# Optimization experiments

Hardware: AMD Instinct MI355X
Metric: run time of the kernel (lower is better)

The kernel has to match this reference:

```python
import jax, jax.numpy as jnp
import numpy as np

V, E, H, L, B, T = 32000, 256, 512, 2, 32, 64
SOS_TOKEN = 1


def setup_inputs() -> dict:
    key = jax.random.key(0)
    ks = jax.random.split(key, 16)
    s = 0.02
    inp = {
        'encoder_outputs': jax.random.normal(ks[0], (B, T, H), dtype=jnp.float32),
        'encoder_hidden': jax.random.normal(ks[1], (L, B, H), dtype=jnp.float32),
        'target_tensor': jax.random.randint(ks[2], (B, T), 0, V, dtype=jnp.int64),
        'embedding': jax.random.normal(ks[3], (V, E), dtype=jnp.float32) * s,
        'W_ih0': jax.random.normal(ks[4], (3 * H, E), dtype=jnp.float32) * s,
        'W_hh0': jax.random.normal(ks[5], (3 * H, H), dtype=jnp.float32) * s,
        'b_ih0': jax.random.normal(ks[6], (3 * H,), dtype=jnp.float32) * s,
        'b_hh0': jax.random.normal(ks[7], (3 * H,), dtype=jnp.float32) * s,
        'W_ih1': jax.random.normal(ks[8], (3 * H, H), dtype=jnp.float32) * s,
        'W_hh1': jax.random.normal(ks[9], (3 * H, H), dtype=jnp.float32) * s,
        'b_ih1': jax.random.normal(ks[10], (3 * H,), dtype=jnp.float32) * s,
        'b_hh1': jax.random.normal(ks[11], (3 * H,), dtype=jnp.float32) * s,
        'W_out': jax.random.normal(ks[12], (V, H), dtype=jnp.float32) * s,
        'b_out': jax.random.normal(ks[13], (V,), dtype=jnp.float32) * s,
    }
    return inp


def gru_cell(x, h, W_ih, W_hh, b_ih, b_hh):
    # PyTorch GRU cell: gates ordered [r, z, n]
    gi = x @ W_ih.T + b_ih            # [B, 3H]
    gh = h @ W_hh.T + b_hh            # [B, 3H]
    i_r, i_z, i_n = jnp.split(gi, 3, axis=-1)
    h_r, h_z, h_n = jnp.split(gh, 3, axis=-1)
    r = jax.nn.sigmoid(i_r + h_r)
    z = jax.nn.sigmoid(i_z + h_z)
    n = jnp.tanh(i_n + r * h_n)
    return (1.0 - z) * n + z * h


def reference(encoder_outputs, encoder_hidden, target_tensor,
              embedding, W_ih0, W_hh0, b_ih0, b_hh0,
              W_ih1, W_hh1, b_ih1, b_hh1, W_out, b_out):
    # full teacher forcing: input token at step i is target[:, i-1], SOS at step 0
    tokens = jnp.concatenate(
        [jnp.full((B, 1), SOS_TOKEN, dtype=target_tensor.dtype),
         target_tensor[:, :-1]], axis=1)                     # [B, T]
    emb = jax.nn.relu(embedding[tokens])                     # [B, T, E]
    emb_t = jnp.swapaxes(emb, 0, 1)                          # [T, B, E]

    def step(h, x):
        h0 = gru_cell(x, h[0], W_ih0, W_hh0, b_ih0, b_hh0)
        h1 = gru_cell(h0, h[1], W_ih1, W_hh1, b_ih1, b_hh1)
        h_new = jnp.stack([h0, h1])                          # [L, B, H]
        return h_new, h1

    h_final, tops = jax.lax.scan(step, encoder_hidden, emb_t)  # tops: [T, B, H]
    logits = jnp.einsum('tbh,vh->btv', tops, W_out) + b_out    # [B, T, V]
    log_probs = jax.nn.log_softmax(logits, axis=-1)
    return log_probs, h_final
```

## Files before the change

### kernel.cpp

```cpp
#include <hip/hip_runtime.h>
#include <hip/hip_bf16.h>

namespace {

constexpr int NV = 32000;
constexpr int NE = 256;
constexpr int NH = 512;
constexpr int NB = 32;
constexpr int NT = 64;
constexpr int NG = 3 * NH;
constexpr int NM = NB * NT;
constexpr int SOS = 1;
constexpr int NTILE = 250;
constexpr int NITEM = 8 * NTILE;
constexpr int NWORK = 232;
constexpr int NV4 = NV / 4;

typedef _Float16 f16_t;
typedef _Float16 f16x8 __attribute__((ext_vector_type(8)));
typedef float f32x4 __attribute__((ext_vector_type(4)));

typedef __attribute__((address_space(1))) void gvoid_t;
typedef __attribute__((address_space(3))) void lvoid_t;

union P8 { f16_t h[4]; unsigned long long u; };

__device__ __forceinline__ int fragoff(int u, int b) {
  return ((b >> 4) * 16 + (u >> 5)) * 512 +
         ((((u >> 3) & 3) * 16) + (b & 15)) * 8 + (u & 7);
}

__device__ __forceinline__ void load_wf(const float* wrow, f16x8* wf) {
  #pragma unroll
  for (int kc = 0; kc < 16; ++kc) {
    f32x4 a = *(const f32x4*)(wrow + kc * 32);
    f32x4 c = *(const f32x4*)(wrow + kc * 32 + 4);
    f16x8 w;
    w[0] = (f16_t)a[0]; w[1] = (f16_t)a[1]; w[2] = (f16_t)a[2]; w[3] = (f16_t)a[3];
    w[4] = (f16_t)c[0]; w[5] = (f16_t)c[1]; w[6] = (f16_t)c[2]; w[7] = (f16_t)c[3];
    wf[kc] = w;
  }
}

__device__ __forceinline__ float sigm(float x) { return 1.f / (1.f + __expf(-x)); }

__device__ __forceinline__ void wait_flag(int* p, int target) {
  while (__hip_atomic_load(p, __ATOMIC_RELAXED, __HIP_MEMORY_SCOPE_AGENT) < target)
    __builtin_amdgcn_s_sleep(1);
}

__device__ __forceinline__ int peek_flag(int* p) {
  return __hip_atomic_load(p, __ATOMIC_RELAXED, __HIP_MEMORY_SCOPE_AGENT);
}

__device__ __forceinline__ void store8(void* dst, unsigned long long v) {
  __hip_atomic_store((unsigned long long*)dst, v, __ATOMIC_RELAXED,
                     __HIP_MEMORY_SCOPE_AGENT);
}


__global__ __launch_bounds__(256) void k_gi0(const int* __restrict__ tgt,
                                             const float* __restrict__ emb,
                                             const float* __restrict__ Wih0,
                                             const float* __restrict__ bih0,
                                             f16_t* __restrict__ Gi0) {
  __shared__ float xs[NE * 33];
  __shared__ int toks[NB];
  const int t = blockIdx.y;
  const int tid = threadIdx.x;
  if (tid < NB) toks[tid] = (t == 0) ? SOS : tgt[tid * NT + (t - 1)];
  __syncthreads();
  #pragma unroll 4
  for (int b = 0; b < NB; ++b) {
    float v = emb[(size_t)toks[b] * NE + tid];
    xs[tid * 33 + b] = v > 0.f ? v : 0.f;
  }
  __syncthreads();
  const int b = tid & 31;
  #pragma unroll
  for (int jj = 0; jj < 8; ++jj) {
    const int j = blockIdx.x * 64 + jj * 8 + (tid >> 5);
    float acc = bih0[j];
    const f32x4* wr = (const f32x4*)(Wih0 + (size_t)j * NE);
    #pragma unroll 4
    for (int e4 = 0; e4 < NE / 4; ++e4) {
      f32x4 w = wr[e4];
      acc += w[0] * xs[(4 * e4 + 0) * 33 + b] + w[1] * xs[(4 * e4 + 1) * 33 + b]
           + w[2] * xs[(4 * e4 + 2) * 33 + b] + w[3] * xs[(4 * e4 + 3) * 33 + b];
    }
    Gi0[((size_t)t * NG + j) * NB + b] = (f16_t)acc;
  }
}


__global__ __launch_bounds__(768) void k_mega(
    const f16_t* __restrict__ Gi0,
    const float* __restrict__ Whh0, const float* __restrict__ bhh0,
    const float* __restrict__ Wih1, const float* __restrict__ bih1,
    const float* __restrict__ Whh1, const float* __restrict__ bhh1,
    const float* __restrict__ eh,
    f16_t* __restrict__ hb0, f16_t* __restrict__ hb1,
    f16_t* __restrict__ Abf, float* __restrict__ hfin,
    const float* __restrict__ Wout, const float* __restrict__ bout,
    f16_t* __restrict__ Wf, float* __restrict__ C,
    float* __restrict__ smax, float* __restrict__ ssum,
    int* f0, int* f1, int* cnt, int* wflag, int* initc) {
  __shared__ __align__(16) char pool[49152];
  __shared__ float red[32];
  __shared__ float mW[256], sW[256];
  const int tid = threadIdx.x;
  const int wave = tid >> 6, lane = tid & 63;
  const int bid = blockIdx.x;
  const int eb = tid & 31, eu0 = (tid >> 5) & 15;

  if (bid < 8) {
    float* gLDS = (float*)pool;
    f16_t* hstage = (f16_t*)(pool + 24576);
    const int ug = bid * 64;
    const int gate = wave >> 2, tile = wave & 3;
    const int row = gate * 512 + ug + tile * 16 + (lane & 15);
    f16x8 wf[16];
    load_wf(Whh0 + (size_t)row * NH + (lane >> 4) * 8, wf);

    for (int k = tid; k < 512; k += 768) {
      const int u0 = ug + (k & 15) * 4, b = k >> 4;
      P8 p;
      #pragma unroll
      for (int i = 0; i < 4; ++i) p.h[i] = (f16_t)eh[b * NH + u0 + i];
      store8(hb0 + fragoff(u0, b), p.u);
    }
    __syncthreads();
    if (tid == 0) {
      __hip_atomic_fetch_add(initc, 1, __ATOMIC_RELEASE, __HIP_MEMORY_SCOPE_AGENT);
      wait_flag(initc, 24);
    }
    __syncthreads();

    float hprev[4], br[4], bz[4], bn[4];
    if (tid < 512) {
      #pragma unroll
      for (int i = 0; i < 4; ++i) {
        int u = ug + eu0 + i * 16;
        hprev[i] = eh[eb * NH + u];
        br[i] = bhh0[u]; bz[i] = bhh0[512 + u]; bn[i] = bhh0[1024 + u];
      }
    }

    for (int t = 0; t < NT; ++t) {
      float gr[4], gz[4], gn[4];
      if (tid < 512) {
        const f16_t* g = Gi0 + (size_t)t * NG * NB;
        #pragma unroll
        for (int i = 0; i < 4; ++i) {
          int u = ug + eu0 + i * 16;
          gr[i] = (float)g[u * NB + eb];
          gz[i] = (float)g[(512 + u) * NB + eb];
          gn[i] = (float)g[(1024 + u) * NB + eb];
        }
      }
      if (t > 0 && tid < 8) wait_flag(f0 + tid * 16, t);
      __syncthreads();
      const f16_t* hb = hb0 + (size_t)t * 16384;
      f32x4 acc0 = {0.f, 0.f, 0.f, 0.f}, acc1 = {0.f, 0.f, 0.f, 0.f};
      #pragma unroll
      for (int kc = 0; kc < 16; ++kc) {
        f16x8 b0 = *(const f16x8*)(hb + kc * 512 + lane * 8);
        f16x8 b1 = *(const f16x8*)(hb + (16 + kc) * 512 + lane * 8);
        acc0 = __builtin_amdgcn_mfma_f32_16x16x32_f16(wf[kc], b0, acc0, 0, 0, 0);
        acc1 = __builtin_amdgcn_mfma_f32_16x16x32_f16(wf[kc], b1, acc1, 0, 0, 0);
      }
      {
        const int m0 = (lane >> 4) * 4, col = lane & 15;
        #pragma unroll
        for (int r = 0; r < 4; ++r) {
          int ul = tile * 16 + m0 + r;
          gLDS[(gate * 64 + ul) * 32 + col] = acc0[r];
          gLDS[(gate * 64 + ul) * 32 + 16 + col] = acc1[r];
        }
      }
      __syncthreads();
      if (tid < 512) {
        #pragma unroll
        for (int i = 0; i < 4; ++i) {
          int ul = eu0 + i * 16;
          float rt = gLDS[(0 * 64 + ul) * 32 + eb];
          float zt = gLDS[(1 * 64 + ul) * 32 + eb];
          float nt_ = gLDS[(2 * 64 + ul) * 32 + eb];
          float r = sigm(gr[i] + rt + br[i]);
          float z = sigm(gz[i] + zt + bz[i]);
          float n = tanhf(gn[i] + r * (nt_ + bn[i]));
          float hnew = (1.f - z) * n + z * hprev[i];
          hprev[i] = hnew;
          hstage[((eb >> 4) * 2 + (ul >> 5)) * 512 +
                 ((((ul >> 3) & 3) * 16) + (eb & 15)) * 8 + (ul & 7)] = (f16_t)hnew;
          if (t == NT - 1) hfin[eb * NH + ug + ul] = hnew;
        }
      }
      __syncthreads();
      if (tid < 512) {
        const int chunk = tid >> 7, w = tid & 127;
        const unsigned long long v =
            *(const unsigned long long*)(hstage + chunk * 512 + w * 4);
        store8(hb0 + (size_t)(t + 1) * 16384 +
               ((chunk >> 1) * 16 + (ug >> 5) + (chunk & 1)) * 512 + w * 4, v);
      }
      __syncthreads();
      if (tid == 0)
        __hip_atomic_store(f0 + bid * 16, t + 1, __ATOMIC_RELEASE,
                           __HIP_MEMORY_SCOPE_AGENT);
    }
  } else if (bid < 24) {
    float* gLDS = (float*)pool;
    f16_t* hstage = (f16_t*)(pool + 24576);
    f16_t* astage = (f16_t*)(pool + 28672);
    const int g = bid - 8, ug = g * 32;
    const int mm = wave >= 6;
    const int w6 = mm ? wave - 6 : wave;
    const int gate = w6 >> 1, tile = w6 & 1;
    const int row = gate * 512 + ug + tile * 16 + (lane & 15);
    const float* W = mm ? Whh1 : Wih1;
    f16x8 wf[16];
    load_wf(W + (size_t)row * NH + (lane >> 4) * 8, wf);

    for (int k = tid; k < 256; k += 768) {
      const int u0 = ug + (k & 7) * 4, b = k >> 3;
      P8 p;
      #pragma unroll
      for (int i = 0; i < 4; ++i) p.h[i] = (f16_t)eh[16384 + b * NH + u0 + i];
      store8(hb1 + fragoff(u0, b), p.u);
    }
    __syncthreads();
    if (tid == 0) {
      __hip_atomic_fetch_add(initc, 1, __ATOMIC_RELEASE, __HIP_MEMORY_SCOPE_AGENT);
      wait_flag(initc, 24);
    }
    __syncthreads();

    float hprev[2], bir[2], biz[2], bin_[2], bhr[2], bhz[2], bhn[2];
    if (tid < 512) {
      #pragma unroll
      for (int i = 0; i < 2; ++i) {
        int u = ug + eu0 + i * 16;
        hprev[i] = eh[16384 + eb * NH + u];
        bir[i] = bih1[u]; biz[i] = bih1[512 + u]; bin_[i] = bih1[1024 + u];
        bhr[i] = bhh1[u]; bhz[i] = bhh1[512 + u]; bhn[i] = bhh1[1024 + u];
      }
    }

    for (int t = 0; t < NT; ++t) {
      if (tid < 24) {
        int* p   = (tid < 8) ? (f0 + tid * 16) : (f1 + (tid - 8) * 16);
        int tgt  = (tid < 8) ? (t + 1) : t;
        wait_flag(p, tgt);
      }
      __syncthreads();
      const f16_t* hb = mm ? (hb1 + (size_t)t * 16384)
                           : (hb0 + (size_t)(t + 1) * 16384);
      f32x4 acc0 = {0.f, 0.f, 0.f, 0.f}, acc1 = {0.f, 0.f, 0.f, 0.f};
      #pragma unroll
      for (int kc = 0; kc < 16; ++kc) {
        f16x8 b0 = *(const f16x8*)(hb + kc * 512 + lane * 8);
        f16x8 b1 = *(const f16x8*)(hb + (16 + kc) * 512 + lane * 8);
        acc0 = __builtin_amdgcn_mfma_f32_16x16x32_f16(wf[kc], b0, acc0, 0, 0, 0);
        acc1 = __builtin_amdgcn_mfma_f32_16x16x32_f16(wf[kc], b1, acc1, 0, 0, 0);
      }
      {
        const int m0 = (lane >> 4) * 4, col = lane & 15;
        #pragma unroll
        for (int r = 0; r < 4; ++r) {
          int ul = tile * 16 + m0 + r;
          gLDS[((mm * 3 + gate) * 32 + ul) * 32 + col] = acc0[r];
          gLDS[((mm * 3 + gate) * 32 + ul) * 32 + 16 + col] = acc1[r];
        }
      }
      __syncthreads();
      if (tid < 512) {
        #pragma unroll
        for (int i = 0; i < 2; ++i) {
          int ul = eu0 + i * 16;
          float ir  = gLDS[((0 * 3 + 0) * 32 + ul) * 32 + eb] + bir[i];
          float iz  = gLDS[((0 * 3 + 1) * 32 + ul) * 32 + eb] + biz[i];
          float in_ = gLDS[((0 * 3 + 2) * 32 + ul) * 32 + eb] + bin_[i];
          float hr  = gLDS[((1 * 3 + 0) * 32 + ul) * 32 + eb] + bhr[i];
          float hz  = gLDS[((1 * 3 + 1) * 32 + ul) * 32 + eb] + bhz[i];
          float hn  = gLDS[((1 * 3 + 2) * 32 + ul) * 32 + eb] + bhn[i];
          float r = sigm(ir + hr);
          float z = sigm(iz + hz);
          float n = tanhf(in_ + r * hn);
          float hnew = (1.f - z) * n + z * hprev[i];
          hprev[i] = hnew;
          f16_t hv = (f16_t)hnew;
          hstage[(eb >> 4) * 512 +
                 ((((ul >> 3) & 3) * 16) + (eb & 15)) * 8 + (ul & 7)] = hv;
          astage[eb * 32 + ul] = hv;
          if (t == NT - 1) hfin[16384 + eb * NH + ug + ul] = hnew;
        }
      }
      __syncthreads();
      if (tid < 256) {
        const int chunk = tid >> 7, w = tid & 127;
        const unsigned long long v =
            *(const unsigned long long*)(hstage + chunk * 512 + w * 4);
        store8(hb1 + (size_t)(t + 1) * 16384 + (chunk * 16 + g) * 512 + w * 4, v);
      } else if (tid < 512) {
        const int i2 = tid - 256;
        const int b = i2 >> 3, uo = (i2 & 7) * 4;
        store8(Abf + ((size_t)(t * NB + b)) * 512 + ug + uo,
               *(const unsigned long long*)(astage + b * 32 + uo));
      }
      __syncthreads();
      if (tid == 0)
        __hip_atomic_store(f1 + g * 16, t + 1, __ATOMIC_RELEASE,
                           __HIP_MEMORY_SCOPE_AGENT);
    }
  } else {
    f16_t* AsB = (f16_t*)pool;
    f16_t* BsB = (f16_t*)(pool + 32768);
    const int wid = bid - 24;
    const int r_in = lane >> 2;
    const int c8 = (lane & 3) * 8;

    auto lsm_row = [&](int idx) {
      const int t = idx >> 5, b = idx & 31;
      float mt = -3.0e38f, st = 0.f;
      if (tid < NTILE) {
        mt = smax[(size_t)idx * NTILE + tid];
        st = ssum[(size_t)idx * NTILE + tid];
      }
      float m = mt;
      #pragma unroll
      for (int o = 1; o < 64; o <<= 1) m = fmaxf(m, __shfl_xor(m, o, 64));
      if (lane == 0) red[wave] = m;
      __syncthreads();
      m = red[0];
      #pragma unroll
      for (int wv = 1; wv < 12; ++wv) m = fmaxf(m, red[wv]);
      float sc = st * __expf(mt - m);
      #pragma unroll
      for (int o = 1; o < 64; o <<= 1) sc += __shfl_xor(sc, o, 64);
      if (lane == 0) red[16 + wave] = sc;
      __syncthreads();
      float S = 0.f;
      #pragma unroll
      for (int wv = 0; wv < 12; ++wv) S += red[16 + wv];
      const float lse = m + __logf(S);
      f32x4* p4 = (f32x4*)(C + (size_t)(b * 64 + t) * NV);
      for (int i = tid; i < NV4; i += 768) {
        f32x4 v = p4[i];
        v[0] -= lse; v[1] -= lse; v[2] -= lse; v[3] -= lse;
        p4[i] = v;
      }
      __syncthreads();
    };

    for (int tl = wid; tl < NTILE; tl += NWORK) {
      for (int i = tid; i < 128 * 512 / 8; i += 768) {
        const float* src = Wout + (size_t)tl * 128 * 512 + i * 8;
        f32x4 a = *(const f32x4*)src;
        f32x4 b = *(const f32x4*)(src + 4);
        f16x8 o;
        o[0] = (f16_t)a[0]; o[1] = (f16_t)a[1]; o[2] = (f16_t)a[2]; o[3] = (f16_t)a[3];
        o[4] = (f16_t)b[0]; o[5] = (f16_t)b[1]; o[6] = (f16_t)b[2]; o[7] = (f16_t)b[3];
        *(f16x8*)(Wf + (size_t)tl * 128 * 512 + i * 8) = o;
      }
      __syncthreads();
      if (tid == 0)
        __hip_atomic_store(wflag + tl * 16, 1, __ATOMIC_RELEASE,
                           __HIP_MEMORY_SCOPE_AGENT);
    }

    int lsmIdx = wid;

    for (int item = wid; item < NITEM; item += NWORK) {
      const int mp = item / NTILE, tl = item - mp * NTILE;
      const int m0 = mp * 256;
      const int n0 = tl * 128;
      if (tid < 16) wait_flag(f1 + tid * 16, mp * 8 + 8);
      else if (tid == 16) wait_flag(wflag + tl * 16, 1);
      __syncthreads();

      auto stage = [&](int buf, int kk) {
        if (wave < 8) {
          const f16_t* Ag = Abf + (size_t)(m0 + wave * 32 + r_in) * NH + kk + c8;
          f16_t* la = AsB + buf * 8192 + (wave * 32) * 32;
          __builtin_amdgcn_global_load_lds((gvoid_t*)Ag, (lvoid_t*)la, 16, 0, 0);
          __builtin_amdgcn_global_load_lds((gvoid_t*)(Ag + 16 * NH),
                                           (lvoid_t*)(la + 16 * 32), 16, 0, 0);
        } else {
          const f16_t* Bg = Wf + (size_t)(n0 + (wave - 8) * 32 + r_in) * NH + kk + c8;
          f16_t* lb = BsB + buf * 4096 + ((wave - 8) * 32) * 32;
          __builtin_amdgcn_global_load_lds((gvoid_t*)Bg, (lvoid_t*)lb, 16, 0, 0);
          __builtin_amdgcn_global_load_lds((gvoid_t*)(Bg + 16 * NH),
                                           (lvoid_t*)(lb + 16 * 32), 16, 0, 0);
        }
      };

      f32x4 acc[4][4];
      #pragma unroll
      for (int i = 0; i < 4; ++i)
        #pragma unroll
        for (int j = 0; j < 4; ++j)
          acc[i][j] = (f32x4){0.f, 0.f, 0.f, 0.f};

      const int wm = (wave >> 1) * 64;
      const int wn = (wave & 1) * 64;
      const int arow = lane & 15;
      const int kg = (lane >> 4) * 8;

      stage(0, 0);
      __syncthreads();
      for (int kt = 0; kt < NH / 32; ++kt) {
        const int buf = kt & 1;
        if (kt + 1 < NH / 32) stage(buf ^ 1, (kt + 1) * 32);
        if (wave < 8) {
          f16x8 af[4], bfr[4];
          #pragma unroll
          for (int i = 0; i < 4; ++i) {
            af[i]  = *(const f16x8*)&AsB[buf * 8192 + (wm + i * 16 + arow) * 32 + kg];
            bfr[i] = *(const f16x8*)&BsB[buf * 4096 + (wn + i * 16 + arow) * 32 + kg];
          }
          #pragma unroll
          for (int i = 0; i < 4; ++i)
            #pragma unroll
            for (int j = 0; j < 4; ++j)
              acc[i][j] = __builtin_amdgcn_mfma_f32_16x16x32_f16(af[i], bfr[j],
                                                                 acc[i][j], 0, 0, 0);
        }
        __syncthreads();
      }

      float myM[4][4], myS[4][4];
      if (wave < 8) {
        const int crow = (lane >> 4) * 4;
        const int ccol = lane & 15;
        float bb[4];
        #pragma unroll
        for (int j = 0; j < 4; ++j) bb[j] = bout[n0 + wn + j * 16 + ccol];
        #pragma unroll
        for (int j = 0; j < 4; ++j) {
          const int gcol = n0 + wn + j * 16 + ccol;
          #pragma unroll
          for (int i = 0; i < 4; ++i) {
            #pragma unroll
            for (int r = 0; r < 4; ++r) {
              const int am = m0 + wm + i * 16 + crow + r;
              const int orow = (am & 31) * 64 + (am >> 5);
              C[(size_t)orow * NV + gcol] = acc[i][j][r] + bb[j];
            }
          }
        }
        #pragma unroll
        for (int i = 0; i < 4; ++i)
          #pragma unroll
          for (int r = 0; r < 4; ++r) {
            float v0 = acc[i][0][r] + bb[0], v1 = acc[i][1][r] + bb[1];
            float v2 = acc[i][2][r] + bb[2], v3 = acc[i][3][r] + bb[3];
            float mm2 = fmaxf(fmaxf(v0, v1), fmaxf(v2, v3));
            #pragma unroll
            for (int o = 1; o < 16; o <<= 1) mm2 = fmaxf(mm2, __shfl_xor(mm2, o, 64));
            float ss = __expf(v0 - mm2) + __expf(v1 - mm2) +
                       __expf(v2 - mm2) + __expf(v3 - mm2);
            #pragma unroll
            for (int o = 1; o < 16; o <<= 1) ss += __shfl_xor(ss, o, 64);
            myM[i][r] = mm2; myS[i][r] = ss;
          }
      }
      __syncthreads();
      if (wave < 8 && (wave & 1) && (lane & 15) == 0) {
        #pragma unroll
        for (int i = 0; i < 4; ++i)
          #pragma unroll
          for (int r = 0; r < 4; ++r) {
            int R = wm + i * 16 + (lane >> 4) * 4 + r;
            mW[R] = myM[i][r]; sW[R] = myS[i][r];
          }
      }
      __syncthreads();
      if (wave < 8 && !(wave & 1) && (lane & 15) == 0) {
        #pragma unroll
        for (int i = 0; i < 4; ++i)
          #pragma unroll
          for (int r = 0; r < 4; ++r) {
            int R = wm + i * 16 + (lane >> 4) * 4 + r;
            float mo = mW[R], so = sW[R];
            float me = myM[i][r], se = myS[i][r];
            float M = fmaxf(me, mo);
            float S = se * __expf(me - M) + so * __expf(mo - M);
            int am = m0 + R;
            smax[(size_t)am * NTILE + tl] = M;
            ssum[(size_t)am * NTILE + tl] = S;
          }
      }
      __syncthreads();
      if (tid == 0)
        __hip_atomic_fetch_add(cnt + mp * 16, 1, __ATOMIC_RELEASE,
                               __HIP_MEMORY_SCOPE_AGENT);

      while (lsmIdx < NM) {
        const int lvl = lsmIdx >> 8;
        if (tid == 0) red[31] = (float)(peek_flag(cnt + lvl * 16) >= NTILE);
        __syncthreads();
        const bool ready = red[31] != 0.f;
        __syncthreads();
        if (!ready) break;
        if (tid == 0) __builtin_amdgcn_fence(__ATOMIC_ACQUIRE, "agent");
        __syncthreads();
        lsm_row(lsmIdx);
        lsmIdx += NWORK;
      }
    }

    for (; lsmIdx < NM; lsmIdx += NWORK) {
      const int lvl = lsmIdx >> 8;
      if (tid == 0) {
        wait_flag(cnt + lvl * 16, NTILE);
        __builtin_amdgcn_fence(__ATOMIC_ACQUIRE, "agent");
      }
      __syncthreads();
      lsm_row(lsmIdx);
    }
  }
}

constexpr size_t WS_F0  = 0;
constexpr size_t WS_F1  = 512;
constexpr size_t WS_CNT = 1536;
constexpr size_t WS_WFL = 2048;
constexpr size_t WS_INI = 18048;
constexpr size_t WS_GI0 = 18432;
constexpr size_t WS_HB0 = WS_GI0 + sizeof(f16_t) * (size_t)NT * NG * NB;
constexpr size_t WS_HB1 = WS_HB0 + sizeof(f16_t) * (size_t)(NT + 1) * NH * NB;
constexpr size_t WS_ABF = WS_HB1 + sizeof(f16_t) * (size_t)(NT + 1) * NH * NB;
constexpr size_t WS_WF  = WS_ABF + sizeof(f16_t) * (size_t)NM * NH;
constexpr size_t WS_SM  = WS_WF + sizeof(f16_t) * (size_t)NV * NH;
constexpr size_t WS_SS  = WS_SM + sizeof(float) * (size_t)NM * NTILE;

}

extern "C" void kernel_launch(void* const* d_in, const int* in_sizes, int n_in,
                              void* d_out, int out_size, void* d_ws, size_t ws_size,
                              hipStream_t stream) {
  const float* enc_h = (const float*)d_in[1];
  const int*   tgt   = (const int*)d_in[2];
  const float* emb   = (const float*)d_in[3];
  const float* Wih0  = (const float*)d_in[4];
  const float* Whh0  = (const float*)d_in[5];
  const float* bih0  = (const float*)d_in[6];
  const float* bhh0  = (const float*)d_in[7];
  const float* Wih1  = (const float*)d_in[8];
  const float* Whh1  = (const float*)d_in[9];
  const float* bih1  = (const float*)d_in[10];
  const float* bhh1  = (const float*)d_in[11];
  const float* Wout  = (const float*)d_in[12];
  const float* bout  = (const float*)d_in[13];

  char* ws = (char*)d_ws;
  int*    f0   = (int*)(ws + WS_F0);
  int*    f1   = (int*)(ws + WS_F1);
  int*    cnt  = (int*)(ws + WS_CNT);
  int*    wfl  = (int*)(ws + WS_WFL);
  int*    ini  = (int*)(ws + WS_INI);
  f16_t*  Gi0  = (f16_t*)(ws + WS_GI0);
  f16_t*  hb0  = (f16_t*)(ws + WS_HB0);
  f16_t*  hb1  = (f16_t*)(ws + WS_HB1);
  f16_t*  Abf  = (f16_t*)(ws + WS_ABF);
  f16_t*  Wf   = (f16_t*)(ws + WS_WF);
  float*  sm   = (float*)(ws + WS_SM);
  float*  ss   = (float*)(ws + WS_SS);

  float* out  = (float*)d_out;
  float* hfin = out + (size_t)NM * NV;

  hipMemsetAsync(ws, 0, 18432, stream);
  k_gi0<<<dim3(NG / 64, NT), 256, 0, stream>>>(tgt, emb, Wih0, bih0, Gi0);
  k_mega<<<256, 768, 0, stream>>>(Gi0, Whh0, bhh0, Wih1, bih1, Whh1, bhh1,
                                  enc_h, hb0, hb1, Abf, hfin, Wout, bout,
                                  Wf, out, sm, ss, f0, f1, cnt, wfl, ini);
}
```

Baseline: 779.0 us.

## Fuse layer-0 input projection into persistent mega kernel with per-timestep flags

Removes the separate k_gi0 launch and computes the layer-0 input-gate projection inside the worker blocks of the persistent kernel. Each timestep's projection is split into 8 chunks spread over the worker blocks, and each chunk signals completion through a per-timestep counter. The recurrent layer-0 blocks wait on that counter before reading Gi0 for step t, so the recurrence can start as soon as early timesteps are ready instead of after a full kernel boundary. In exchange, the worker blocks run this projection before their logits work, and the recurrence adds another flag wait per step.

```diff
diff --git a/kernel.cpp b/kernel.cpp
--- a/kernel.cpp
+++ b/kernel.cpp
@@ -59,42 +59,10 @@
 }
 
 
-__global__ __launch_bounds__(256) void k_gi0(const int* __restrict__ tgt,
-                                             const float* __restrict__ emb,
-                                             const float* __restrict__ Wih0,
-                                             const float* __restrict__ bih0,
-                                             f16_t* __restrict__ Gi0) {
-  __shared__ float xs[NE * 33];
-  __shared__ int toks[NB];
-  const int t = blockIdx.y;
-  const int tid = threadIdx.x;
-  if (tid < NB) toks[tid] = (t == 0) ? SOS : tgt[tid * NT + (t - 1)];
-  __syncthreads();
-  #pragma unroll 4
-  for (int b = 0; b < NB; ++b) {
-    float v = emb[(size_t)toks[b] * NE + tid];
-    xs[tid * 33 + b] = v > 0.f ? v : 0.f;
-  }
-  __syncthreads();
-  const int b = tid & 31;
-  #pragma unroll
-  for (int jj = 0; jj < 8; ++jj) {
-    const int j = blockIdx.x * 64 + jj * 8 + (tid >> 5);
-    float acc = bih0[j];
-    const f32x4* wr = (const f32x4*)(Wih0 + (size_t)j * NE);
-    #pragma unroll 4
-    for (int e4 = 0; e4 < NE / 4; ++e4) {
-      f32x4 w = wr[e4];
-      acc += w[0] * xs[(4 * e4 + 0) * 33 + b] + w[1] * xs[(4 * e4 + 1) * 33 + b]
-           + w[2] * xs[(4 * e4 + 2) * 33 + b] + w[3] * xs[(4 * e4 + 3) * 33 + b];
-    }
-    Gi0[((size_t)t * NG + j) * NB + b] = (f16_t)acc;
-  }
-}
-
-
 __global__ __launch_bounds__(768) void k_mega(
-    const f16_t* __restrict__ Gi0,
+    const int* __restrict__ tgt, const float* __restrict__ emb,
+    const float* __restrict__ Wih0, const float* __restrict__ bih0,
+    f16_t* __restrict__ Gi0,
     const float* __restrict__ Whh0, const float* __restrict__ bhh0,
     const float* __restrict__ Wih1, const float* __restrict__ bih1,
     const float* __restrict__ Whh1, const float* __restrict__ bhh1,
@@ -104,10 +72,11 @@
     const float* __restrict__ Wout, const float* __restrict__ bout,
     f16_t* __restrict__ Wf, float* __restrict__ C,
     float* __restrict__ smax, float* __restrict__ ssum,
-    int* f0, int* f1, int* cnt, int* wflag, int* initc) {
+    int* f0, int* f1, int* cnt, int* wflag, int* initc, int* gfl) {
   __shared__ __align__(16) char pool[49152];
   __shared__ float red[32];
   __shared__ float mW[256], sW[256];
+  __shared__ int tks[NB];
   const int tid = threadIdx.x;
   const int wave = tid >> 6, lane = tid & 63;
   const int bid = blockIdx.x;
@@ -147,6 +116,9 @@
     }
 
     for (int t = 0; t < NT; ++t) {
+      if (t > 0 && tid < 8) wait_flag(f0 + tid * 16, t);
+      if (tid == 8) wait_flag(gfl + t * 16, 8);
+      __syncthreads();
       float gr[4], gz[4], gn[4];
       if (tid < 512) {
         const f16_t* g = Gi0 + (size_t)t * NG * NB;
@@ -158,8 +130,6 @@
           gn[i] = (float)g[(1024 + u) * NB + eb];
         }
       }
-      if (t > 0 && tid < 8) wait_flag(f0 + tid * 16, t);
-      __syncthreads();
       const f16_t* hb = hb0 + (size_t)t * 16384;
       f32x4 acc0 = {0.f, 0.f, 0.f, 0.f}, acc1 = {0.f, 0.f, 0.f, 0.f};
       #pragma unroll
@@ -250,8 +220,8 @@
     for (int t = 0; t < NT; ++t) {
       if (tid < 24) {
         int* p   = (tid < 8) ? (f0 + tid * 16) : (f1 + (tid - 8) * 16);
-        int tgt  = (tid < 8) ? (t + 1) : t;
-        wait_flag(p, tgt);
+        int tgt2 = (tid < 8) ? (t + 1) : t;
+        wait_flag(p, tgt2);
       }
       __syncthreads();
       const f16_t* hb = mm ? (hb1 + (size_t)t * 16384)
@@ -320,6 +290,41 @@
     const int r_in = lane >> 2;
     const int c8 = (lane & 3) * 8;
 
+    {
+      float* xs = (float*)pool;
+      for (int it = wid; it < 512; it += NWORK) {
+        const int t = it >> 3, js = (it & 7) * 192;
+        if (tid < NB) tks[tid] = (t == 0) ? SOS : tgt[tid * NT + (t - 1)];
+        __syncthreads();
+        if (tid < NE) {
+          #pragma unroll 4
+          for (int b = 0; b < NB; ++b) {
+            float v = emb[(size_t)tks[b] * NE + tid];
+            xs[tid * 33 + b] = v > 0.f ? v : 0.f;
+          }
+        }
+        __syncthreads();
+        const int b = tid & 31, jrow = tid >> 5;
+        #pragma unroll
+        for (int p = 0; p < 8; ++p) {
+          const int j = js + p * 24 + jrow;
+          float acc = bih0[j];
+          const f32x4* wr = (const f32x4*)(Wih0 + (size_t)j * NE);
+          #pragma unroll 4
+          for (int e4 = 0; e4 < NE / 4; ++e4) {
+            f32x4 w = wr[e4];
+            acc += w[0] * xs[(4 * e4 + 0) * 33 + b] + w[1] * xs[(4 * e4 + 1) * 33 + b]
+                 + w[2] * xs[(4 * e4 + 2) * 33 + b] + w[3] * xs[(4 * e4 + 3) * 33 + b];
+          }
+          Gi0[((size_t)t * NG + j) * NB + b] = (f16_t)acc;
+        }
+        __syncthreads();
+        if (tid == 0)
+          __hip_atomic_fetch_add(gfl + t * 16, 1, __ATOMIC_RELEASE,
+                                 __HIP_MEMORY_SCOPE_AGENT);
+      }
+    }
+
     auto lsm_row = [&](int idx) {
       const int t = idx >> 5, b = idx & 31;
       float mt = -3.0e38f, st = 0.f;
@@ -527,7 +532,9 @@
 constexpr size_t WS_CNT = 1536;
 constexpr size_t WS_WFL = 2048;
 constexpr size_t WS_INI = 18048;
-constexpr size_t WS_GI0 = 18432;
+constexpr size_t WS_GFL = 18112;
+constexpr size_t WS_MS0 = 22528;
+constexpr size_t WS_GI0 = 22528;
 constexpr size_t WS_HB0 = WS_GI0 + sizeof(f16_t) * (size_t)NT * NG * NB;
 constexpr size_t WS_HB1 = WS_HB0 + sizeof(f16_t) * (size_t)(NT + 1) * NH * NB;
 constexpr size_t WS_ABF = WS_HB1 + sizeof(f16_t) * (size_t)(NT + 1) * NH * NB;
@@ -560,6 +567,7 @@
   int*    cnt  = (int*)(ws + WS_CNT);
   int*    wfl  = (int*)(ws + WS_WFL);
   int*    ini  = (int*)(ws + WS_INI);
+  int*    gfl  = (int*)(ws + WS_GFL);
   f16_t*  Gi0  = (f16_t*)(ws + WS_GI0);
   f16_t*  hb0  = (f16_t*)(ws + WS_HB0);
   f16_t*  hb1  = (f16_t*)(ws + WS_HB1);
@@ -571,9 +579,9 @@
   float* out  = (float*)d_out;
   float* hfin = out + (size_t)NM * NV;
 
-  hipMemsetAsync(ws, 0, 18432, stream);
-  k_gi0<<<dim3(NG / 64, NT), 256, 0, stream>>>(tgt, emb, Wih0, bih0, Gi0);
-  k_mega<<<256, 768, 0, stream>>>(Gi0, Whh0, bhh0, Wih1, bih1, Whh1, bhh1,
+  hipMemsetAsync(ws, 0, WS_MS0, stream);
+  k_mega<<<256, 768, 0, stream>>>(tgt, emb, Wih0, bih0, Gi0,
+                                  Whh0, bhh0, Wih1, bih1, Whh1, bhh1,
                                   enc_h, hb0, hb1, Abf, hfin, Wout, bout,
-                                  Wf, out, sm, ss, f0, f1, cnt, wfl, ini);
-}
+                                  Wf, out, sm, ss, f0, f1, cnt, wfl, ini, gfl);
+}
```

Result: faster. 708.9 us (median of 2 runs) (-9.0%).
